# Kernel tuning notes

Measured on AMD Instinct MI355X. Metric: run time of the kernel, lower is better.

## Reference

```python
import jax, jax.numpy as jnp
import numpy as np

B = 8          # batch (one decode token per sequence)
H = 16         # query heads
HKV = 8        # kv heads (GQA)
G = H // HKV   # query heads per kv head
D = 128        # head_dim
HID = H * D    # 2048 hidden
VOCAB = 32000
BS = 16        # block_size
MAXB = 256     # blocks per sequence
NBLK = B * MAXB  # total cache blocks
L = MAXB * BS    # max context length = 4096


def setup_inputs() -> dict:
    key = jax.random.key(0)
    ks = jax.random.split(key, 12)
    w = 0.02
    return {
        "tokens": jax.random.randint(ks[0], (B,), 0, VOCAB),
        "positions": jax.random.randint(ks[1], (B,), 0, L - 1),
        "block_table": jnp.arange(B * MAXB, dtype=jnp.int32).reshape(B, MAXB),
        "k_cache": jax.random.normal(ks[2], (NBLK, BS, HKV, D), jnp.float32),
        "v_cache": jax.random.normal(ks[3], (NBLK, BS, HKV, D), jnp.float32),
        "embed": jax.random.normal(ks[4], (VOCAB, HID), jnp.float32) * w,
        "Wq": jax.random.normal(ks[5], (HID, HID), jnp.float32) * w,
        "Wk": jax.random.normal(ks[6], (HID, HKV * D), jnp.float32) * w,
        "Wv": jax.random.normal(ks[7], (HID, HKV * D), jnp.float32) * w,
        "Wo": jax.random.normal(ks[8], (HID, HID), jnp.float32) * w,
        "Wlm": jax.random.normal(ks[9], (HID, VOCAB), jnp.float32) * w,
    }


def reference(tokens, positions, block_table, k_cache, v_cache,
              embed, Wq, Wk, Wv, Wo, Wlm):
    # embed + projections for the single new token per sequence
    xf = embed[tokens]                                   # [B, HID]
    q = (xf @ Wq).reshape(B, HKV, G, D)                  # grouped-query layout
    k_new = (xf @ Wk).reshape(B, HKV, D)
    v_new = (xf @ Wv).reshape(B, HKV, D)

    # paged cache update: scatter new k/v into block_table[b, pos//BS] at offset pos%BS
    slot = block_table[jnp.arange(B), positions // BS] * BS + positions % BS  # [B]
    kc = k_cache.reshape(NBLK * BS, HKV, D).at[slot].set(k_new)
    vc = v_cache.reshape(NBLK * BS, HKV, D).at[slot].set(v_new)

    # paged decode: gather each sequence's KV via its block table
    idx = (block_table[:, :, None] * BS + jnp.arange(BS)[None, None, :]).reshape(B, L)
    kg = kc[idx]                                         # [B, L, HKV, D]
    vg = vc[idx]                                         # [B, L, HKV, D]

    scale = 1.0 / jnp.sqrt(jnp.float32(D))
    scores = jnp.einsum('bgcd,blgd->bgcl', q, kg) * scale  # [B, HKV, G, L]
    valid = jnp.arange(L)[None, :] <= positions[:, None]   # cache_seqlens + 1 tokens valid
    scores = jnp.where(valid[:, None, None, :], scores, -jnp.inf)
    attn = jax.nn.softmax(scores, axis=-1)
    attn_out = jnp.einsum('bgcl,blgd->bgcd', attn, vg).reshape(B, HID)

    out = attn_out @ Wo                                  # o_proj
    logits = (xf + out) @ Wlm                            # residual + lm_head
    return logits                                        # [B, VOCAB]
```

## Files before the change

### kernel.cpp

```cpp
#include <hip/hip_runtime.h>
#include <cstdint>
#include <cstddef>

constexpr int B_    = 8;
constexpr int HKV_  = 8;
constexpr int G_    = 2;
constexpr int D_    = 128;
constexpr int HID_  = 2048;
constexpr int VOCAB_= 32000;
constexpr int BS_   = 16;
constexpr int MAXB_ = 256;
constexpr int L_    = 4096;

constexpr int KSP_QKV = 32;  constexpr int CK_QKV = HID_ / KSP_QKV;
constexpr int KSP_O   = 32;
constexpr int KSP_LM  = 16;  constexpr int CK_LM  = HID_ / KSP_LM;
constexpr int CHUNK   = 128; constexpr int NCHUNK = L_ / CHUNK;
constexpr int NCOL_QKV = HID_ + 1024 + 1024;

constexpr size_t OFF_PQKV = 0;
constexpr size_t OFF_QB   = OFF_PQKV + (size_t)KSP_QKV*B_*NCOL_QKV;
constexpr size_t OFF_KNV  = OFF_QB   + (size_t)B_*HID_;
constexpr size_t OFF_PM   = OFF_KNV  + (size_t)B_*HKV_*2*D_;
constexpr size_t OFF_PL   = OFF_PM   + (size_t)B_*HKV_*NCHUNK*G_;
constexpr size_t OFF_PACC = OFF_PL   + (size_t)B_*HKV_*NCHUNK*G_;
constexpr size_t OFF_PO   = OFF_PACC + (size_t)B_*HKV_*NCHUNK*G_*D_;
constexpr size_t OFF_PLM  = OFF_PO   + (size_t)KSP_O*B_*HID_;

typedef float f32x4_t __attribute__((ext_vector_type(4)));
__device__ __forceinline__ float4 ntload4(const float* p) {
    f32x4_t v = __builtin_nontemporal_load((const f32x4_t*)p);
    return make_float4(v.x, v.y, v.z, v.w);
}
__device__ __forceinline__ float ntload1(const float* p) {
    return __builtin_nontemporal_load(p);
}

__global__ __launch_bounds__(256) void k_qkv_part(const int* __restrict__ tokens,
        const float* __restrict__ embed,
        const float* __restrict__ Wq, const float* __restrict__ Wk,
        const float* __restrict__ Wv, float* __restrict__ pout) {
    __shared__ float xs[CK_QKV * 8];
    const int c  = blockIdx.y;
    const int k0 = c * CK_QKV;
    const int n  = blockIdx.x * 256 + threadIdx.x;
    for (int idx = threadIdx.x; idx < CK_QKV*8; idx += 256) {
        int b = idx >> 6, kk = idx & (CK_QKV-1);
        xs[kk*8 + b] = embed[(size_t)tokens[b]*HID_ + k0 + kk];
    }
    const float* Wp; int stride, col;
    if (n < HID_)            { Wp = Wq; stride = HID_; col = n; }
    else if (n < HID_+1024)  { Wp = Wk; stride = 1024; col = n - HID_; }
    else                     { Wp = Wv; stride = 1024; col = n - HID_ - 1024; }
    __syncthreads();
    float acc[8] = {0,0,0,0,0,0,0,0};
    const float* wp = Wp + (size_t)k0 * stride + col;
    #pragma unroll 16
    for (int kk = 0; kk < CK_QKV; ++kk) {
        float w = ntload1(wp); wp += stride;
        float4 x0 = *(const float4*)&xs[kk*8];
        float4 x1 = *(const float4*)&xs[kk*8 + 4];
        acc[0] += x0.x*w; acc[1] += x0.y*w; acc[2] += x0.z*w; acc[3] += x0.w*w;
        acc[4] += x1.x*w; acc[5] += x1.y*w; acc[6] += x1.z*w; acc[7] += x1.w*w;
    }
    float* po = pout + (size_t)c * 8 * NCOL_QKV + n;
    #pragma unroll
    for (int b = 0; b < 8; ++b) po[(size_t)b*NCOL_QKV] = acc[b];
}

__global__ __launch_bounds__(256) void k_qkv_comb(const float* __restrict__ pqkv,
        float* __restrict__ qb, float* __restrict__ knv) {
    const int tg = blockIdx.x*256 + threadIdx.x;
    const float4* pq4 = (const float4*)pqkv;
    const float scale = 0.08838834764831845f;
    if (tg < 4096) {
        const int b = tg >> 9, c4 = tg & 511;
        float4 s = make_float4(0.f,0.f,0.f,0.f);
        for (int cc = 0; cc < KSP_QKV; ++cc) {
            float4 p = pq4[(size_t)(cc*8 + b)*(NCOL_QKV/4) + c4];
            s.x += p.x; s.y += p.y; s.z += p.z; s.w += p.w;
        }
        s.x*=scale; s.y*=scale; s.z*=scale; s.w*=scale;
        ((float4*)qb)[(size_t)b*512 + c4] = s;
    } else {
        const int u2 = tg - 4096;
        const int b = u2 >> 9, r = u2 & 511;
        const int hkv = r >> 6, j = r & 63;
        const size_t cb4 = (j < 32) ? (size_t)(512 + hkv*32 + j)
                                    : (size_t)(768 + hkv*32 + (j - 32));
        float4 s = make_float4(0.f,0.f,0.f,0.f);
        for (int cc = 0; cc < KSP_QKV; ++cc) {
            float4 p = pq4[(size_t)(cc*8 + b)*(NCOL_QKV/4) + cb4];
            s.x += p.x; s.y += p.y; s.z += p.z; s.w += p.w;
        }
        ((float4*)knv)[(size_t)(b*8 + hkv)*64 + j] = s;
    }
}

__global__ __launch_bounds__(256) void k_attn(const float* __restrict__ qb,
        const float* __restrict__ knv,
        const float* __restrict__ kc, const float* __restrict__ vc,
        const int* __restrict__ positions, const int* __restrict__ btab,
        float* __restrict__ pm, float* __restrict__ pl, float* __restrict__ pacc) {
    const int ch = blockIdx.x, hkv = blockIdx.y, b = blockIdx.z;
    const int pos = positions[b];
    const int c0  = ch * CHUNK;
    const size_t pbase = (size_t)(b*HKV_ + hkv)*NCHUNK + ch;
    const int t = threadIdx.x;
    if (c0 > pos) {
        if (t < 2) { pm[pbase*2 + t] = -1e30f; pl[pbase*2 + t] = 0.f; }
        pacc[pbase*256 + t] = 0.f;
        return;
    }
    const bool haspos = (pos < c0 + CHUNK);

    __shared__ int   bts[CHUNK/BS_];
    __shared__ float acc_l[8][256];
    __shared__ float ml_l[8][2][2];

    if (t < CHUNK/BS_) bts[t] = btab[b*MAXB_ + ch*(CHUNK/BS_) + t];
    __syncthreads();

    const int hw = t >> 5, l32 = t & 31;
    const float4* qb4  = (const float4*)qb;
    const float4* knv4 = (const float4*)knv;
    float4 q0 = qb4[(size_t)b*512 + hkv*64 + l32];
    float4 q1 = qb4[(size_t)b*512 + hkv*64 + 32 + l32];

    float m0 = -1e30f, m1 = -1e30f, l0 = 0.f, l1 = 0.f;
    float a0[4] = {0,0,0,0}, a1[4] = {0,0,0,0};

    #pragma unroll 8
    for (int i = 0; i < CHUNK/8; ++i) {
        const int lo = i*8 + hw;
        const int l  = c0 + lo;
        const bool valid = (l < pos);
        size_t row = (size_t)bts[lo >> 4] * BS_ + (lo & (BS_-1));
        size_t off = (row*HKV_ + hkv)*D_ + l32*4;
        float4 kv = ntload4(kc + off);
        float4 vv = ntload4(vc + off);
        float s0 = q0.x*kv.x + q0.y*kv.y + q0.z*kv.z + q0.w*kv.w;
        float s1 = q1.x*kv.x + q1.y*kv.y + q1.z*kv.z + q1.w*kv.w;
        #pragma unroll
        for (int m = 16; m >= 1; m >>= 1) { s0 += __shfl_xor(s0, m); s1 += __shfl_xor(s1, m); }
        if (!valid) { s0 = -1e30f; s1 = -1e30f; }
        float nm0 = fmaxf(m0, s0);
        float cr0 = __expf(m0 - nm0);
        float p0  = valid ? __expf(s0 - nm0) : 0.f;
        m0 = nm0; l0 = l0*cr0 + p0;
        a0[0] = a0[0]*cr0 + p0*vv.x; a0[1] = a0[1]*cr0 + p0*vv.y;
        a0[2] = a0[2]*cr0 + p0*vv.z; a0[3] = a0[3]*cr0 + p0*vv.w;
        float nm1 = fmaxf(m1, s1);
        float cr1 = __expf(m1 - nm1);
        float p1  = valid ? __expf(s1 - nm1) : 0.f;
        m1 = nm1; l1 = l1*cr1 + p1;
        a1[0] = a1[0]*cr1 + p1*vv.x; a1[1] = a1[1]*cr1 + p1*vv.y;
        a1[2] = a1[2]*cr1 + p1*vv.z; a1[3] = a1[3]*cr1 + p1*vv.w;
    }

    if (haspos && hw == 0) {
        float4 kv = knv4[(size_t)(b*8 + hkv)*64 + l32];
        float4 vv = knv4[(size_t)(b*8 + hkv)*64 + 32 + l32];
        float s0 = q0.x*kv.x + q0.y*kv.y + q0.z*kv.z + q0.w*kv.w;
        float s1 = q1.x*kv.x + q1.y*kv.y + q1.z*kv.z + q1.w*kv.w;
        #pragma unroll
        for (int m = 16; m >= 1; m >>= 1) { s0 += __shfl_xor(s0, m); s1 += __shfl_xor(s1, m); }
        float nm0 = fmaxf(m0, s0);
        float cr0 = __expf(m0 - nm0);
        float p0  = __expf(s0 - nm0);
        m0 = nm0; l0 = l0*cr0 + p0;
        a0[0] = a0[0]*cr0 + p0*vv.x; a0[1] = a0[1]*cr0 + p0*vv.y;
        a0[2] = a0[2]*cr0 + p0*vv.z; a0[3] = a0[3]*cr0 + p0*vv.w;
        float nm1 = fmaxf(m1, s1);
        float cr1 = __expf(m1 - nm1);
        float p1  = __expf(s1 - nm1);
        m1 = nm1; l1 = l1*cr1 + p1;
        a1[0] = a1[0]*cr1 + p1*vv.x; a1[1] = a1[1]*cr1 + p1*vv.y;
        a1[2] = a1[2]*cr1 + p1*vv.z; a1[3] = a1[3]*cr1 + p1*vv.w;
    }

    *(float4*)&acc_l[hw][0*D_ + l32*4] = make_float4(a0[0],a0[1],a0[2],a0[3]);
    *(float4*)&acc_l[hw][1*D_ + l32*4] = make_float4(a1[0],a1[1],a1[2],a1[3]);
    if (l32 == 0) {
        ml_l[hw][0][0] = m0; ml_l[hw][0][1] = l0;
        ml_l[hw][1][0] = m1; ml_l[hw][1][1] = l1;
    }
    __syncthreads();

    const int g = t >> 7, d = t & 127;
    float M = -1e30f;
    #pragma unroll
    for (int h = 0; h < 8; ++h) M = fmaxf(M, ml_l[h][g][0]);
    float Ls = 0.f, val = 0.f;
    #pragma unroll
    for (int h = 0; h < 8; ++h) {
        float w = __expf(ml_l[h][g][0] - M);
        Ls  += w * ml_l[h][g][1];
        val += w * acc_l[h][g*D_ + d];
    }
    pacc[pbase*256 + t] = val;
    if (d == 0) { pm[pbase*2 + g] = M; pl[pbase*2 + g] = Ls; }
}

__global__ __launch_bounds__(256) void k_o_part(const float* __restrict__ pm,
        const float* __restrict__ pl, const float* __restrict__ pacc,
        const float* __restrict__ Wo, float* __restrict__ po) {
    const int cb   = blockIdx.y;
    const int head = cb >> 1;
    const int hkv  = head >> 1, g = head & 1;
    const int dhalf = (cb & 1) * 64;
    const int t = threadIdx.x;
    const int n = blockIdx.x * 256 + t;

    __shared__ float pms[8][NCHUNK], pls[8][NCHUNK];
    __shared__ float wch[8][NCHUNK];
    __shared__ float wsum[8];
    __shared__ float xs[64 * 8];

    {
        int bb = t >> 5, ch = t & 31;
        size_t ix = ((size_t)(bb*HKV_ + hkv)*NCHUNK + ch)*2 + g;
        pms[bb][ch] = pm[ix];
        pls[bb][ch] = pl[ix];
    }
    __syncthreads();
    if (t < 8) {
        float M = -1e30f;
        for (int ch = 0; ch < NCHUNK; ++ch) M = fmaxf(M, pms[t][ch]);
        float Ls = 0.f;
        for (int ch = 0; ch < NCHUNK; ++ch) {
            float w = __expf(pms[t][ch] - M);
            wch[t][ch] = w;
            Ls += w * pls[t][ch];
        }
        wsum[t] = 1.f / Ls;
    }
    __syncthreads();
    if (t < 128) {
        int bb = t >> 4, j = t & 15;
        float4 a = make_float4(0.f,0.f,0.f,0.f);
        size_t base4 = ((size_t)(bb*HKV_ + hkv)*NCHUNK)*64 + (size_t)(g*128 + dhalf)/4 + j;
        for (int ch = 0; ch < NCHUNK; ++ch) {
            float w = wch[bb][ch];
            float4 p = ((const float4*)pacc)[base4 + (size_t)ch*64];
            a.x += w*p.x; a.y += w*p.y; a.z += w*p.z; a.w += w*p.w;
        }
        float inv = wsum[bb];
        xs[(j*4+0)*8 + bb] = a.x*inv;
        xs[(j*4+1)*8 + bb] = a.y*inv;
        xs[(j*4+2)*8 + bb] = a.z*inv;
        xs[(j*4+3)*8 + bb] = a.w*inv;
    }
    __syncthreads();

    float acc[8] = {0,0,0,0,0,0,0,0};
    const float* wp = Wo + (size_t)(head*D_ + dhalf) * HID_ + n;
    #pragma unroll 16
    for (int kk = 0; kk < 64; ++kk) {
        float w = ntload1(wp); wp += HID_;
        float4 x0 = *(const float4*)&xs[kk*8];
        float4 x1 = *(const float4*)&xs[kk*8 + 4];
        acc[0] += x0.x*w; acc[1] += x0.y*w; acc[2] += x0.z*w; acc[3] += x0.w*w;
        acc[4] += x1.x*w; acc[5] += x1.y*w; acc[6] += x1.z*w; acc[7] += x1.w*w;
    }
    #pragma unroll
    for (int b = 0; b < 8; ++b) po[((size_t)cb*8 + b)*HID_ + n] = acc[b];
}

__global__ __launch_bounds__(256) void k_lm_part(const int* __restrict__ tokens,
        const float* __restrict__ embed, const float* __restrict__ po,
        const float* __restrict__ Wlm, float* __restrict__ plm) {
    __shared__ float xs[CK_LM * 8];
    const int c  = blockIdx.y;
    const int k0 = c * CK_LM;
    const int t  = threadIdx.x;
    {
        int bb = t >> 5, j = t & 31;
        size_t col4 = (size_t)(k0 >> 2) + j;
        float4 a = ((const float4*)embed)[(size_t)tokens[bb]*(HID_/4) + col4];
        for (int c2 = 0; c2 < KSP_O; ++c2) {
            float4 p = ((const float4*)po)[(size_t)(c2*8 + bb)*(HID_/4) + col4];
            a.x += p.x; a.y += p.y; a.z += p.z; a.w += p.w;
        }
        xs[(j*4+0)*8 + bb] = a.x;
        xs[(j*4+1)*8 + bb] = a.y;
        xs[(j*4+2)*8 + bb] = a.z;
        xs[(j*4+3)*8 + bb] = a.w;
    }
    __syncthreads();

    const int n0 = blockIdx.x * 1024 + t * 4;
    if (n0 >= VOCAB_) return;
    float4 acc[8];
    #pragma unroll
    for (int b = 0; b < 8; ++b) acc[b] = make_float4(0.f,0.f,0.f,0.f);
    const float* wp = Wlm + (size_t)k0 * VOCAB_ + n0;
    #pragma unroll 16
    for (int kk = 0; kk < CK_LM; ++kk) {
        float4 w = *(const float4*)wp; wp += VOCAB_;
        float4 x0 = *(const float4*)&xs[kk*8];
        float4 x1 = *(const float4*)&xs[kk*8 + 4];
        acc[0].x += x0.x*w.x; acc[0].y += x0.x*w.y; acc[0].z += x0.x*w.z; acc[0].w += x0.x*w.w;
        acc[1].x += x0.y*w.x; acc[1].y += x0.y*w.y; acc[1].z += x0.y*w.z; acc[1].w += x0.y*w.w;
        acc[2].x += x0.z*w.x; acc[2].y += x0.z*w.y; acc[2].z += x0.z*w.z; acc[2].w += x0.z*w.w;
        acc[3].x += x0.w*w.x; acc[3].y += x0.w*w.y; acc[3].z += x0.w*w.z; acc[3].w += x0.w*w.w;
        acc[4].x += x1.x*w.x; acc[4].y += x1.x*w.y; acc[4].z += x1.x*w.z; acc[4].w += x1.x*w.w;
        acc[5].x += x1.y*w.x; acc[5].y += x1.y*w.y; acc[5].z += x1.y*w.z; acc[5].w += x1.y*w.w;
        acc[6].x += x1.z*w.x; acc[6].y += x1.z*w.y; acc[6].z += x1.z*w.z; acc[6].w += x1.z*w.w;
        acc[7].x += x1.w*w.x; acc[7].y += x1.w*w.y; acc[7].z += x1.w*w.z; acc[7].w += x1.w*w.w;
    }
    #pragma unroll
    for (int b = 0; b < 8; ++b)
        *(float4*)&plm[(size_t)(c*8 + b)*VOCAB_ + n0] = acc[b];
}

__global__ __launch_bounds__(256) void k_lm_comb(const float* __restrict__ plm,
                                                 float* __restrict__ out) {
    const int b = blockIdx.y;
    const int n4 = blockIdx.x * 256 + threadIdx.x;
    if (n4 >= VOCAB_/4) return;
    float4 s = make_float4(0.f,0.f,0.f,0.f);
    #pragma unroll
    for (int c = 0; c < KSP_LM; ++c) {
        float4 p = ((const float4*)plm)[(size_t)(c*8 + b)*(VOCAB_/4) + n4];
        s.x += p.x; s.y += p.y; s.z += p.z; s.w += p.w;
    }
    ((float4*)out)[(size_t)b*(VOCAB_/4) + n4] = s;
}

extern "C" void kernel_launch(void* const* d_in, const int* in_sizes, int n_in,
                              void* d_out, int out_size, void* d_ws, size_t ws_size,
                              hipStream_t stream) {
    const int*   tokens    = (const int*)  d_in[0];
    const int*   positions = (const int*)  d_in[1];
    const int*   btab      = (const int*)  d_in[2];
    const float* kc        = (const float*)d_in[3];
    const float* vc        = (const float*)d_in[4];
    const float* embed     = (const float*)d_in[5];
    const float* Wq        = (const float*)d_in[6];
    const float* Wk        = (const float*)d_in[7];
    const float* Wv        = (const float*)d_in[8];
    const float* Wo        = (const float*)d_in[9];
    const float* Wlm       = (const float*)d_in[10];
    float* out = (float*)d_out;
    float* ws  = (float*)d_ws;

    float* pqkv = ws + OFF_PQKV;
    float* qb   = ws + OFF_QB;
    float* knv  = ws + OFF_KNV;
    float* pm   = ws + OFF_PM;
    float* pl   = ws + OFF_PL;
    float* pacc = ws + OFF_PACC;
    float* po   = ws + OFF_PO;
    float* plm  = ws + OFF_PLM;

    k_qkv_part<<<dim3(NCOL_QKV/256, KSP_QKV), 256, 0, stream>>>(tokens, embed, Wq, Wk, Wv, pqkv);
    k_qkv_comb<<<32, 256, 0, stream>>>(pqkv, qb, knv);
    k_attn    <<<dim3(NCHUNK, HKV_, B_), 256, 0, stream>>>(qb, knv, kc, vc, positions, btab,
                                                           pm, pl, pacc);
    k_o_part  <<<dim3(HID_/256, KSP_O), 256, 0, stream>>>(pm, pl, pacc, Wo, po);
    k_lm_part <<<dim3((VOCAB_ + 1023)/1024, KSP_LM), 256, 0, stream>>>(tokens, embed, po, Wlm, plm);
    k_lm_comb <<<dim3((VOCAB_/4 + 255)/256, B_), 256, 0, stream>>>(plm, out);
}
```

Baseline: 112.5 us.

## Restructure paged attention: one warp per kv head over 32-token chunks

The attention kernel now gives each 32-lane group a different kv head and walks 32 consecutive tokens per block, instead of 8 warps striding over a 128-token chunk of one head. The in-block shared-memory merge is dropped, and each warp writes its own partial max, sum and accumulator straight to global memory. The new-token k/v is folded into the main loop by pointer selection rather than handled in a separate tail. The cost is four times more partials for the o_proj combine kernel to read and reduce, plus a serial 32-step dependency chain per warp.

New measurement: 123.6 us. 1.1x slower.

```diff
diff --git a/kernel.cpp b/kernel.cpp
--- a/kernel.cpp
+++ b/kernel.cpp
@@ -15,17 +15,17 @@
 constexpr int KSP_QKV = 32;  constexpr int CK_QKV = HID_ / KSP_QKV;
 constexpr int KSP_O   = 32;
 constexpr int KSP_LM  = 16;  constexpr int CK_LM  = HID_ / KSP_LM;
-constexpr int CHUNK   = 128; constexpr int NCHUNK = L_ / CHUNK;
+constexpr int ACH     = 32;  constexpr int NACH   = L_ / ACH;
 constexpr int NCOL_QKV = HID_ + 1024 + 1024;
 
 constexpr size_t OFF_PQKV = 0;
 constexpr size_t OFF_QB   = OFF_PQKV + (size_t)KSP_QKV*B_*NCOL_QKV;
 constexpr size_t OFF_KNV  = OFF_QB   + (size_t)B_*HID_;
 constexpr size_t OFF_PM   = OFF_KNV  + (size_t)B_*HKV_*2*D_;
-constexpr size_t OFF_PL   = OFF_PM   + (size_t)B_*HKV_*NCHUNK*G_;
-constexpr size_t OFF_PACC = OFF_PL   + (size_t)B_*HKV_*NCHUNK*G_;
-constexpr size_t OFF_PO   = OFF_PACC + (size_t)B_*HKV_*NCHUNK*G_*D_;
-constexpr size_t OFF_PLM  = OFF_PO   + (size_t)KSP_O*B_*HID_;
+constexpr size_t OFF_PL   = OFF_PM   + (size_t)B_*HKV_*NACH*G_;
+constexpr size_t OFF_PACC = OFF_PL   + (size_t)B_*HKV_*NACH*G_;
+constexpr size_t OFF_PO   = OFF_PACC + (size_t)B_*HKV_*NACH*G_*D_;
+constexpr size_t OFF_PLM  = OFF_PO   + (size_t)32*B_*HID_;
 
 typedef float f32x4_t __attribute__((ext_vector_type(4)));
 __device__ __forceinline__ float4 ntload4(const float* p) {
@@ -102,26 +102,24 @@
         const float* __restrict__ kc, const float* __restrict__ vc,
         const int* __restrict__ positions, const int* __restrict__ btab,
         float* __restrict__ pm, float* __restrict__ pl, float* __restrict__ pacc) {
-    const int ch = blockIdx.x, hkv = blockIdx.y, b = blockIdx.z;
+    const int ch = blockIdx.x, b = blockIdx.y;
     const int pos = positions[b];
-    const int c0  = ch * CHUNK;
-    const size_t pbase = (size_t)(b*HKV_ + hkv)*NCHUNK + ch;
+    const int c0  = ch * ACH;
     const int t = threadIdx.x;
+    const int hkv = t >> 5, l32 = t & 31;
+    const size_t pbase = (size_t)((b*HKV_ + hkv)*NACH + ch);
     if (c0 > pos) {
-        if (t < 2) { pm[pbase*2 + t] = -1e30f; pl[pbase*2 + t] = 0.f; }
-        pacc[pbase*256 + t] = 0.f;
+        if (l32 < 2) { pm[pbase*2 + l32] = -1e30f; pl[pbase*2 + l32] = 0.f; }
+        #pragma unroll
+        for (int g = 0; g < 2; ++g)
+            *(float4*)&pacc[pbase*256 + g*128 + l32*4] = make_float4(0.f,0.f,0.f,0.f);
         return;
     }
-    const bool haspos = (pos < c0 + CHUNK);
-
-    __shared__ int   bts[CHUNK/BS_];
-    __shared__ float acc_l[8][256];
-    __shared__ float ml_l[8][2][2];
-
-    if (t < CHUNK/BS_) bts[t] = btab[b*MAXB_ + ch*(CHUNK/BS_) + t];
-    __syncthreads();
-
-    const int hw = t >> 5, l32 = t & 31;
+
+    __shared__ int bts[ACH/BS_];
+    if (t < ACH/BS_) bts[t] = btab[b*MAXB_ + ch*(ACH/BS_) + t];
+    __syncthreads();
+
     const float4* qb4  = (const float4*)qb;
     const float4* knv4 = (const float4*)knv;
     float4 q0 = qb4[(size_t)b*512 + hkv*64 + l32];
@@ -131,14 +129,20 @@
     float a0[4] = {0,0,0,0}, a1[4] = {0,0,0,0};
 
     #pragma unroll 8
-    for (int i = 0; i < CHUNK/8; ++i) {
-        const int lo = i*8 + hw;
-        const int l  = c0 + lo;
-        const bool valid = (l < pos);
-        size_t row = (size_t)bts[lo >> 4] * BS_ + (lo & (BS_-1));
-        size_t off = (row*HKV_ + hkv)*D_ + l32*4;
-        float4 kv = ntload4(kc + off);
-        float4 vv = ntload4(vc + off);
+    for (int i = 0; i < ACH; ++i) {
+        const int l = c0 + i;
+        const bool valid = (l <= pos);
+        const float *kp, *vp;
+        if (l == pos) {
+            kp = (const float*)&knv4[(size_t)(b*8 + hkv)*64 + l32];
+            vp = (const float*)&knv4[(size_t)(b*8 + hkv)*64 + 32 + l32];
+        } else {
+            size_t row = (size_t)bts[i >> 4] * BS_ + (i & (BS_-1));
+            size_t off = row*(HKV_*D_) + hkv*D_ + l32*4;
+            kp = kc + off;  vp = vc + off;
+        }
+        float4 kv = ntload4(kp);
+        float4 vv = ntload4(vp);
         float s0 = q0.x*kv.x + q0.y*kv.y + q0.z*kv.z + q0.w*kv.w;
         float s1 = q1.x*kv.x + q1.y*kv.y + q1.z*kv.z + q1.w*kv.w;
         #pragma unroll
@@ -158,48 +162,12 @@
         a1[2] = a1[2]*cr1 + p1*vv.z; a1[3] = a1[3]*cr1 + p1*vv.w;
     }
 
-    if (haspos && hw == 0) {
-        float4 kv = knv4[(size_t)(b*8 + hkv)*64 + l32];
-        float4 vv = knv4[(size_t)(b*8 + hkv)*64 + 32 + l32];
-        float s0 = q0.x*kv.x + q0.y*kv.y + q0.z*kv.z + q0.w*kv.w;
-        float s1 = q1.x*kv.x + q1.y*kv.y + q1.z*kv.z + q1.w*kv.w;
-        #pragma unroll
-        for (int m = 16; m >= 1; m >>= 1) { s0 += __shfl_xor(s0, m); s1 += __shfl_xor(s1, m); }
-        float nm0 = fmaxf(m0, s0);
-        float cr0 = __expf(m0 - nm0);
-        float p0  = __expf(s0 - nm0);
-        m0 = nm0; l0 = l0*cr0 + p0;
-        a0[0] = a0[0]*cr0 + p0*vv.x; a0[1] = a0[1]*cr0 + p0*vv.y;
-        a0[2] = a0[2]*cr0 + p0*vv.z; a0[3] = a0[3]*cr0 + p0*vv.w;
-        float nm1 = fmaxf(m1, s1);
-        float cr1 = __expf(m1 - nm1);
-        float p1  = __expf(s1 - nm1);
-        m1 = nm1; l1 = l1*cr1 + p1;
-        a1[0] = a1[0]*cr1 + p1*vv.x; a1[1] = a1[1]*cr1 + p1*vv.y;
-        a1[2] = a1[2]*cr1 + p1*vv.z; a1[3] = a1[3]*cr1 + p1*vv.w;
-    }
-
-    *(float4*)&acc_l[hw][0*D_ + l32*4] = make_float4(a0[0],a0[1],a0[2],a0[3]);
-    *(float4*)&acc_l[hw][1*D_ + l32*4] = make_float4(a1[0],a1[1],a1[2],a1[3]);
+    *(float4*)&pacc[pbase*256 +   0 + l32*4] = make_float4(a0[0],a0[1],a0[2],a0[3]);
+    *(float4*)&pacc[pbase*256 + 128 + l32*4] = make_float4(a1[0],a1[1],a1[2],a1[3]);
     if (l32 == 0) {
-        ml_l[hw][0][0] = m0; ml_l[hw][0][1] = l0;
-        ml_l[hw][1][0] = m1; ml_l[hw][1][1] = l1;
-    }
-    __syncthreads();
-
-    const int g = t >> 7, d = t & 127;
-    float M = -1e30f;
-    #pragma unroll
-    for (int h = 0; h < 8; ++h) M = fmaxf(M, ml_l[h][g][0]);
-    float Ls = 0.f, val = 0.f;
-    #pragma unroll
-    for (int h = 0; h < 8; ++h) {
-        float w = __expf(ml_l[h][g][0] - M);
-        Ls  += w * ml_l[h][g][1];
-        val += w * acc_l[h][g*D_ + d];
-    }
-    pacc[pbase*256 + t] = val;
-    if (d == 0) { pm[pbase*2 + g] = M; pl[pbase*2 + g] = Ls; }
+        pm[pbase*2 + 0] = m0; pl[pbase*2 + 0] = l0;
+        pm[pbase*2 + 1] = m1; pl[pbase*2 + 1] = l1;
+    }
 }
 
 __global__ __launch_bounds__(256) void k_o_part(const float* __restrict__ pm,
@@ -212,23 +180,27 @@
     const int t = threadIdx.x;
     const int n = blockIdx.x * 256 + t;
 
-    __shared__ float pms[8][NCHUNK], pls[8][NCHUNK];
-    __shared__ float wch[8][NCHUNK];
+    __shared__ float pms[8][NACH], pls[8][NACH];
+    __shared__ float wch[8][NACH];
     __shared__ float wsum[8];
     __shared__ float xs[64 * 8];
 
     {
-        int bb = t >> 5, ch = t & 31;
-        size_t ix = ((size_t)(bb*HKV_ + hkv)*NCHUNK + ch)*2 + g;
-        pms[bb][ch] = pm[ix];
-        pls[bb][ch] = pl[ix];
+        #pragma unroll
+        for (int r = 0; r < 4; ++r) {
+            int id = t + r*256;
+            int bb = id >> 7, ch = id & 127;
+            size_t ix = ((size_t)(bb*HKV_ + hkv)*NACH + ch)*2 + g;
+            pms[bb][ch] = pm[ix];
+            pls[bb][ch] = pl[ix];
+        }
     }
     __syncthreads();
     if (t < 8) {
         float M = -1e30f;
-        for (int ch = 0; ch < NCHUNK; ++ch) M = fmaxf(M, pms[t][ch]);
+        for (int ch = 0; ch < NACH; ++ch) M = fmaxf(M, pms[t][ch]);
         float Ls = 0.f;
-        for (int ch = 0; ch < NCHUNK; ++ch) {
+        for (int ch = 0; ch < NACH; ++ch) {
             float w = __expf(pms[t][ch] - M);
             wch[t][ch] = w;
             Ls += w * pls[t][ch];
@@ -239,8 +211,8 @@
     if (t < 128) {
         int bb = t >> 4, j = t & 15;
         float4 a = make_float4(0.f,0.f,0.f,0.f);
-        size_t base4 = ((size_t)(bb*HKV_ + hkv)*NCHUNK)*64 + (size_t)(g*128 + dhalf)/4 + j;
-        for (int ch = 0; ch < NCHUNK; ++ch) {
+        size_t base4 = ((size_t)(bb*HKV_ + hkv)*NACH)*64 + (size_t)(g*128 + dhalf)/4 + j;
+        for (int ch = 0; ch < NACH; ++ch) {
             float w = wch[bb][ch];
             float4 p = ((const float4*)pacc)[base4 + (size_t)ch*64];
             a.x += w*p.x; a.y += w*p.y; a.z += w*p.z; a.w += w*p.w;
@@ -278,7 +250,7 @@
         int bb = t >> 5, j = t & 31;
         size_t col4 = (size_t)(k0 >> 2) + j;
         float4 a = ((const float4*)embed)[(size_t)tokens[bb]*(HID_/4) + col4];
-        for (int c2 = 0; c2 < KSP_O; ++c2) {
+        for (int c2 = 0; c2 < 32; ++c2) {
             float4 p = ((const float4*)po)[(size_t)(c2*8 + bb)*(HID_/4) + col4];
             a.x += p.x; a.y += p.y; a.z += p.z; a.w += p.w;
         }
@@ -356,9 +328,9 @@
 
     k_qkv_part<<<dim3(NCOL_QKV/256, KSP_QKV), 256, 0, stream>>>(tokens, embed, Wq, Wk, Wv, pqkv);
     k_qkv_comb<<<32, 256, 0, stream>>>(pqkv, qb, knv);
-    k_attn    <<<dim3(NCHUNK, HKV_, B_), 256, 0, stream>>>(qb, knv, kc, vc, positions, btab,
-                                                           pm, pl, pacc);
-    k_o_part  <<<dim3(HID_/256, KSP_O), 256, 0, stream>>>(pm, pl, pacc, Wo, po);
+    k_attn    <<<dim3(NACH, B_), 256, 0, stream>>>(qb, knv, kc, vc, positions, btab,
+                                                   pm, pl, pacc);
+    k_o_part  <<<dim3(HID_/256, 32), 256, 0, stream>>>(pm, pl, pacc, Wo, po);
     k_lm_part <<<dim3((VOCAB_ + 1023)/1024, KSP_LM), 256, 0, stream>>>(tokens, embed, po, Wlm, plm);
     k_lm_comb <<<dim3((VOCAB_/4 + 255)/256, B_), 256, 0, stream>>>(plm, out);
 }
```
